# Kernel tuning notes

Hardware: AMD Instinct MI355X
Metric: run time of the kernel (lower is better)

## Reference

```python
import jax, jax.numpy as jnp
import numpy as np

BS, SEQ, DIM, DIM_MLP, E = 2, 2048, 1024, 4096, 8
STD = 0.02  # nn.init.normal_(weight, std=0.02)


def setup_inputs() -> dict:
    key = jax.random.key(0)
    k_x, k_idx, k_w1, k_w2 = jax.random.split(key, 4)
    x = jax.random.normal(k_x, (BS, SEQ, DIM), dtype=jnp.float32)
    expert_idx = jax.random.randint(k_idx, (BS, SEQ), 0, E, dtype=jnp.int32)
    W1 = jax.random.normal(k_w1, (E, DIM, DIM_MLP), dtype=jnp.float32) * STD
    b1 = jnp.zeros((E, DIM_MLP), dtype=jnp.float32)
    W2 = jax.random.normal(k_w2, (E, DIM_MLP, DIM), dtype=jnp.float32) * STD
    b2 = jnp.zeros((E, DIM), dtype=jnp.float32)
    return {"x": x, "expert_idx": expert_idx, "W1": W1, "b1": b1, "W2": W2, "b2": b2}


def reference(x, expert_idx, W1, b1, W2, b2):
    # Compute ALL experts on all tokens (faithful to the torch module).
    # h: [bs, seq, E, dim_mlp]
    h = jnp.einsum("bsd,edm->bsem", x, W1) + b1
    h = jax.nn.gelu(h, approximate=False)  # torch nn.GELU default = exact erf
    # feat: [bs, seq, E, dim]  (== torch.cat along feature dim, reshaped)
    feat = jnp.einsum("bsem,emd->bsed", h, W2) + b2
    # Per-token gather of the assigned expert's output (top-1 select).
    idx = expert_idx.astype(jnp.int32)[:, :, None, None]  # [bs, seq, 1, 1]
    out = jnp.take_along_axis(feat, idx, axis=2)[:, :, 0, :]  # [bs, seq, dim]
    return out
```

## Files before the change

kernel.cpp:

```cpp
#include <hip/hip_runtime.h>
#include <hip/hip_bf16.h>
#include <math.h>

#define TOK   4096
#define DIM   1024
#define DMLP  4096
#define NE    8
#define BM    128
#define BN    128
#define BN2   64
#define BK    64
#define PADMAX (TOK + NE * BM)
#define NTILES (PADMAX / BM)

typedef __attribute__((ext_vector_type(8))) short  short8;
typedef __attribute__((ext_vector_type(4))) float  float4v;
typedef __attribute__((ext_vector_type(4))) unsigned short ushort4v;

#define ASYNC16(gp, lp) __builtin_amdgcn_global_load_lds( \
    (const __attribute__((address_space(1))) unsigned int*)(gp), \
    (__attribute__((address_space(3))) unsigned int*)(lp), 16, 0, 0)

#define FRAG_OFF(R, C) (((((R) << 3) + ((C) ^ ((R) & 7)))) << 3)

static __device__ __forceinline__ unsigned short f2bf(float f) {
  unsigned u = __float_as_uint(f);
  u += 0x7fffu + ((u >> 16) & 1u);
  return (unsigned short)(u >> 16);
}

__global__ void group_kernel(const int* __restrict__ eidx,
                             int* __restrict__ perm,
                             int* __restrict__ tile_e) {
  __shared__ int cnt[NE], off[NE], len[NE], cur[NE];
  const int tid = threadIdx.x;
  if (tid < NE) cnt[tid] = 0;
  __syncthreads();
  for (int i = tid; i < TOK; i += 256) atomicAdd(&cnt[eidx[i]], 1);
  __syncthreads();
  if (tid == 0) {
    int o = 0;
    for (int e = 0; e < NE; e++) {
      off[e] = o;
      len[e] = ((cnt[e] + BM - 1) / BM) * BM;
      cur[e] = o;
      o += len[e];
    }
  }
  __syncthreads();
  for (int s = tid; s < PADMAX; s += 256) perm[s] = -1;
  __syncthreads();
  for (int i = tid; i < TOK; i += 256) {
    const int e = eidx[i];
    const int p = atomicAdd(&cur[e], 1);
    perm[p] = i;
  }
  __syncthreads();
  for (int t = tid; t < NTILES; t += 256) {
    const int row = t * BM;
    int te = -1;
    for (int e = 0; e < NE; e++)
      if (row >= off[e] && row < off[e] + len[e]) te = e;
    tile_e[t] = te;
  }
}

__global__ __launch_bounds__(256)
void convtrans_kernel(const float* __restrict__ W, unsigned short* __restrict__ WT,
                      int K, int N) {
  __shared__ unsigned short T[64][66];
  const int e  = blockIdx.z;
  const int k0 = blockIdx.y * 64, n0 = blockIdx.x * 64;
  const float* Win = W + (size_t)e * K * N;
  unsigned short* Wout = WT + (size_t)e * K * N;
  const int tid = threadIdx.x;
  const int nl  = tid & 63;
  const int kb  = (tid >> 6) * 16;
#pragma unroll
  for (int r = 0; r < 16; r++) {
    const int kl = kb + r;
    T[nl][kl] = f2bf(Win[(size_t)(k0 + kl) * N + n0 + nl]);
  }
  __syncthreads();
  const int kc = (tid & 31) * 2;
  const int nb = tid >> 5;
#pragma unroll
  for (int r = 0; r < 8; r++) {
    const int nl2 = nb + r * 8;
    const unsigned v = *(const unsigned*)&T[nl2][kc];
    *(unsigned*)&Wout[(size_t)(n0 + nl2) * K + k0 + kc] = v;
  }
}

__global__ __launch_bounds__(256)
void xgather_kernel(const float* __restrict__ x, const int* __restrict__ perm,
                    unsigned short* __restrict__ xg) {
  const int slot = blockIdx.x;
  const int t    = perm[slot];
  const int tid  = threadIdx.x;
  ushort4v o = (ushort4v){0, 0, 0, 0};
  if (t >= 0) {
    const float4v v = *(const float4v*)(x + (size_t)t * DIM + tid * 4);
#pragma unroll
    for (int q = 0; q < 4; q++) o[q] = f2bf(v[q]);
  }
  *(ushort4v*)(xg + (size_t)slot * DIM + tid * 4) = o;
}

__global__ __launch_bounds__(256)
void gemm1_kernel(const unsigned short* __restrict__ xg,
                  const unsigned short* __restrict__ W1T,
                  const float* __restrict__ b1, const int* __restrict__ tile_e,
                  unsigned short* __restrict__ h) {
  const int te = tile_e[blockIdx.x];
  if (te < 0) return;
  const unsigned short* Asrc = xg + (size_t)blockIdx.x * BM * DIM;
  const unsigned short* Bsrc = W1T + (size_t)te * DIM * DMLP + (size_t)(blockIdx.y * BN) * DIM;
  const int tid = threadIdx.x;

  __shared__ __align__(16) unsigned short As[BM * BK];
  __shared__ __align__(16) unsigned short Bs[BN * BK];

  const unsigned short* ag[4];
  const unsigned short* bg[4];
  int lo[4];
#pragma unroll
  for (int t = 0; t < 4; t++) {
    const int p = t * 256 + tid;
    const int r = p >> 3;
    const int c = (p & 7) ^ (r & 7);
    ag[t] = Asrc + (size_t)r * DIM + c * 8;
    bg[t] = Bsrc + (size_t)r * DIM + c * 8;
    lo[t] = p * 8;
  }

  const int wid = tid >> 6, lane = tid & 63;
  const int wm = (wid >> 1) * 64, wn = (wid & 1) * 64;
  const int l15 = lane & 15, quad = lane >> 4;

  float4v acc[4][4];
#pragma unroll
  for (int i = 0; i < 4; i++)
#pragma unroll
    for (int j = 0; j < 4; j++) acc[i][j] = (float4v){0.f, 0.f, 0.f, 0.f};

  for (int k0 = 0; k0 < DIM; k0 += BK) {
#pragma unroll
    for (int t = 0; t < 4; t++) ASYNC16(ag[t] + k0, &As[lo[t]]);
#pragma unroll
    for (int t = 0; t < 4; t++) ASYNC16(bg[t] + k0, &Bs[lo[t]]);
    __syncthreads();

#pragma unroll
    for (int hh = 0; hh < 2; hh++) {
      short8 a[4], b[4];
      const int C = hh * 4 + quad;
#pragma unroll
      for (int i = 0; i < 4; i++) a[i] = *(const short8*)&As[FRAG_OFF(wm + i * 16 + l15, C)];
#pragma unroll
      for (int j = 0; j < 4; j++) b[j] = *(const short8*)&Bs[FRAG_OFF(wn + j * 16 + l15, C)];
#pragma unroll
      for (int i = 0; i < 4; i++)
#pragma unroll
        for (int j = 0; j < 4; j++)
          acc[i][j] = __builtin_amdgcn_mfma_f32_16x16x32_bf16(a[i], b[j], acc[i][j], 0, 0, 0);
    }
    __syncthreads();
  }

#pragma unroll
  for (int i = 0; i < 4; i++) {
#pragma unroll
    for (int j = 0; j < 4; j++) {
      const int col = blockIdx.y * BN + wn + j * 16 + l15;
      const float bias = b1[te * DMLP + col];
#pragma unroll
      for (int r = 0; r < 4; r++) {
        const int row = wm + i * 16 + quad * 4 + r;
        float v = acc[i][j][r] + bias;
        v = 0.5f * v * (1.0f + erff(v * 0.7071067811865475f));
        h[(size_t)(blockIdx.x * BM + row) * DMLP + col] = f2bf(v);
      }
    }
  }
}

__global__ __launch_bounds__(256)
void gemm2_kernel(const unsigned short* __restrict__ h,
                  const unsigned short* __restrict__ W2T,
                  const float* __restrict__ b2, const int* __restrict__ perm,
                  const int* __restrict__ tile_e, float* __restrict__ out) {
  const int te = tile_e[blockIdx.x];
  if (te < 0) return;
  const unsigned short* Asrc = h + (size_t)blockIdx.x * BM * DMLP;
  const unsigned short* Bsrc = W2T + (size_t)te * DMLP * DIM + (size_t)(blockIdx.y * BN2) * DMLP;
  const int tid = threadIdx.x;

  __shared__ __align__(16) unsigned short As[BM * BK];
  __shared__ __align__(16) unsigned short Bs[BN2 * BK];

  const unsigned short* ag[4];
  const unsigned short* bg[2];
  int alo[4], blo[2];
#pragma unroll
  for (int t = 0; t < 4; t++) {
    const int p = t * 256 + tid;
    const int r = p >> 3;
    const int c = (p & 7) ^ (r & 7);
    ag[t] = Asrc + (size_t)r * DMLP + c * 8;
    alo[t] = p * 8;
  }
#pragma unroll
  for (int t = 0; t < 2; t++) {
    const int p = t * 256 + tid;
    const int r = p >> 3;
    const int c = (p & 7) ^ (r & 7);
    bg[t] = Bsrc + (size_t)r * DMLP + c * 8;
    blo[t] = p * 8;
  }

  const int wid = tid >> 6, lane = tid & 63;
  const int wm = (wid >> 1) * 64, wn = (wid & 1) * 32;
  const int l15 = lane & 15, quad = lane >> 4;

  float4v acc[4][2];
#pragma unroll
  for (int i = 0; i < 4; i++)
#pragma unroll
    for (int j = 0; j < 2; j++) acc[i][j] = (float4v){0.f, 0.f, 0.f, 0.f};

  for (int k0 = 0; k0 < DMLP; k0 += BK) {
#pragma unroll
    for (int t = 0; t < 4; t++) ASYNC16(ag[t] + k0, &As[alo[t]]);
#pragma unroll
    for (int t = 0; t < 2; t++) ASYNC16(bg[t] + k0, &Bs[blo[t]]);
    __syncthreads();

#pragma unroll
    for (int hh = 0; hh < 2; hh++) {
      short8 a[4], b[2];
      const int C = hh * 4 + quad;
#pragma unroll
      for (int i = 0; i < 4; i++) a[i] = *(const short8*)&As[FRAG_OFF(wm + i * 16 + l15, C)];
#pragma unroll
      for (int j = 0; j < 2; j++) b[j] = *(const short8*)&Bs[FRAG_OFF(wn + j * 16 + l15, C)];
#pragma unroll
      for (int i = 0; i < 4; i++)
#pragma unroll
        for (int j = 0; j < 2; j++)
          acc[i][j] = __builtin_amdgcn_mfma_f32_16x16x32_bf16(a[i], b[j], acc[i][j], 0, 0, 0);
    }
    __syncthreads();
  }

#pragma unroll
  for (int i = 0; i < 4; i++) {
#pragma unroll
    for (int j = 0; j < 2; j++) {
      const int col = blockIdx.y * BN2 + wn + j * 16 + l15;
      const float bias = b2[te * DIM + col];
#pragma unroll
      for (int r = 0; r < 4; r++) {
        const int row  = wm + i * 16 + quad * 4 + r;
        const int slot = blockIdx.x * BM + row;
        const int t    = perm[slot];
        if (t >= 0) out[(size_t)t * DIM + col] = acc[i][j][r] + bias;
      }
    }
  }
}

extern "C" void kernel_launch(void* const* d_in, const int* in_sizes, int n_in,
                              void* d_out, int out_size, void* d_ws, size_t ws_size,
                              hipStream_t stream) {
  const float* x    = (const float*)d_in[0];
  const int*   eidx = (const int*)d_in[1];
  const float* W1   = (const float*)d_in[2];
  const float* b1   = (const float*)d_in[3];
  const float* W2   = (const float*)d_in[4];
  const float* b2   = (const float*)d_in[5];
  float* out = (float*)d_out;

  char* ws = (char*)d_ws;
  int* perm   = (int*)ws;
  int* tile_e = (int*)(ws + PADMAX * sizeof(int));
  unsigned short* xg  = (unsigned short*)(ws + 32768);
  unsigned short* h   = (unsigned short*)(ws + 32768 + 10485760);
  unsigned short* W1T = (unsigned short*)(ws + 32768 + 10485760 + 41943040);
  unsigned short* W2T = (unsigned short*)((char*)W1T + 67108864);

  group_kernel<<<1, 256, 0, stream>>>(eidx, perm, tile_e);
  convtrans_kernel<<<dim3(DMLP / 64, DIM / 64, NE), 256, 0, stream>>>(W1, W1T, DIM, DMLP);
  convtrans_kernel<<<dim3(DIM / 64, DMLP / 64, NE), 256, 0, stream>>>(W2, W2T, DMLP, DIM);
  xgather_kernel<<<PADMAX, 256, 0, stream>>>(x, perm, xg);
  gemm1_kernel<<<dim3(NTILES, DMLP / BN), 256, 0, stream>>>(xg, W1T, b1, tile_e, h);
  gemm2_kernel<<<dim3(NTILES, DIM / BN2), 256, 0, stream>>>(h, W2T, b2, perm, tile_e, out);
}
```

Measured before the change: 494.0 us.

## Pack weights in k8-blocked layout, double-buffer GEMM LDS loads, swap grid order

Replaces the transpose-through-LDS weight conversion with a vectorized pack kernel that writes bf16 weights in [K/8][N][8] blocked order, so the GEMM B-tile loads read contiguous 16-byte chunks. Both GEMMs now double-buffer the A and B tiles in LDS, issuing the next tile's async loads before computing on the current one, with one barrier per iteration. The grid is reordered so consecutive blocks share the same token tile and expert, which should improve L2 reuse of A and the expert weights. The cost is twice the LDS use per block, which may lower occupancy.

```diff
diff --git a/kernel.cpp b/kernel.cpp
--- a/kernel.cpp
+++ b/kernel.cpp
@@ -66,29 +66,22 @@
 }
 
 __global__ __launch_bounds__(256)
-void convtrans_kernel(const float* __restrict__ W, unsigned short* __restrict__ WT,
-                      int K, int N) {
-  __shared__ unsigned short T[64][66];
+void convpack_kernel(const float* __restrict__ W, unsigned short* __restrict__ WT,
+                     int K, int N) {
   const int e  = blockIdx.z;
-  const int k0 = blockIdx.y * 64, n0 = blockIdx.x * 64;
-  const float* Win = W + (size_t)e * K * N;
-  unsigned short* Wout = WT + (size_t)e * K * N;
-  const int tid = threadIdx.x;
-  const int nl  = tid & 63;
-  const int kb  = (tid >> 6) * 16;
-#pragma unroll
-  for (int r = 0; r < 16; r++) {
-    const int kl = kb + r;
-    T[nl][kl] = f2bf(Win[(size_t)(k0 + kl) * N + n0 + nl]);
-  }
-  __syncthreads();
-  const int kc = (tid & 31) * 2;
-  const int nb = tid >> 5;
-#pragma unroll
-  for (int r = 0; r < 8; r++) {
-    const int nl2 = nb + r * 8;
-    const unsigned v = *(const unsigned*)&T[nl2][kc];
-    *(unsigned*)&Wout[(size_t)(n0 + nl2) * K + k0 + kc] = v;
+  const int kg = blockIdx.y;
+  const int n0 = blockIdx.x * 1024 + threadIdx.x * 4;
+  const float* Win = W + (size_t)e * K * N + (size_t)kg * 8 * N + n0;
+  unsigned short* Wout = WT + (size_t)e * K * N + ((size_t)kg * N + n0) * 8;
+  float4v v[8];
+#pragma unroll
+  for (int j = 0; j < 8; j++) v[j] = *(const float4v*)(Win + (size_t)j * N);
+#pragma unroll
+  for (int q = 0; q < 4; q++) {
+    short8 g;
+#pragma unroll
+    for (int j = 0; j < 8; j++) g[j] = (short)f2bf(v[j][q]);
+    *(short8*)(Wout + q * 8) = g;
   }
 }
 
@@ -112,14 +105,16 @@
                   const unsigned short* __restrict__ W1T,
                   const float* __restrict__ b1, const int* __restrict__ tile_e,
                   unsigned short* __restrict__ h) {
-  const int te = tile_e[blockIdx.x];
+  const int bt = blockIdx.y;
+  const int te = tile_e[bt];
   if (te < 0) return;
-  const unsigned short* Asrc = xg + (size_t)blockIdx.x * BM * DIM;
-  const unsigned short* Bsrc = W1T + (size_t)te * DIM * DMLP + (size_t)(blockIdx.y * BN) * DIM;
+  const int n0 = blockIdx.x * BN;
+  const unsigned short* Asrc = xg + (size_t)bt * BM * DIM;
+  const unsigned short* Bsrc = W1T + (size_t)te * DIM * DMLP;
   const int tid = threadIdx.x;
 
-  __shared__ __align__(16) unsigned short As[BM * BK];
-  __shared__ __align__(16) unsigned short Bs[BN * BK];
+  __shared__ __align__(16) unsigned short As[2][BM * BK];
+  __shared__ __align__(16) unsigned short Bs[2][BN * BK];
 
   const unsigned short* ag[4];
   const unsigned short* bg[4];
@@ -130,7 +125,7 @@
     const int r = p >> 3;
     const int c = (p & 7) ^ (r & 7);
     ag[t] = Asrc + (size_t)r * DIM + c * 8;
-    bg[t] = Bsrc + (size_t)r * DIM + c * 8;
+    bg[t] = Bsrc + ((size_t)c * DMLP + n0 + r) * 8;
     lo[t] = p * 8;
   }
 
@@ -144,45 +139,66 @@
 #pragma unroll
     for (int j = 0; j < 4; j++) acc[i][j] = (float4v){0.f, 0.f, 0.f, 0.f};
 
-  for (int k0 = 0; k0 < DIM; k0 += BK) {
-#pragma unroll
-    for (int t = 0; t < 4; t++) ASYNC16(ag[t] + k0, &As[lo[t]]);
-#pragma unroll
-    for (int t = 0; t < 4; t++) ASYNC16(bg[t] + k0, &Bs[lo[t]]);
-    __syncthreads();
-
-#pragma unroll
-    for (int hh = 0; hh < 2; hh++) {
-      short8 a[4], b[4];
-      const int C = hh * 4 + quad;
-#pragma unroll
-      for (int i = 0; i < 4; i++) a[i] = *(const short8*)&As[FRAG_OFF(wm + i * 16 + l15, C)];
-#pragma unroll
-      for (int j = 0; j < 4; j++) b[j] = *(const short8*)&Bs[FRAG_OFF(wn + j * 16 + l15, C)];
-#pragma unroll
-      for (int i = 0; i < 4; i++)
-#pragma unroll
-        for (int j = 0; j < 4; j++)
-          acc[i][j] = __builtin_amdgcn_mfma_f32_16x16x32_bf16(a[i], b[j], acc[i][j], 0, 0, 0);
-    }
-    __syncthreads();
-  }
+#define COMPUTE1(buf)                                                          \
+  do {                                                                         \
+    _Pragma("unroll")                                                          \
+    for (int hh = 0; hh < 2; hh++) {                                           \
+      short8 a[4], b[4];                                                       \
+      const int C = hh * 4 + quad;                                             \
+      _Pragma("unroll")                                                        \
+      for (int i = 0; i < 4; i++)                                              \
+        a[i] = *(const short8*)&As[buf][FRAG_OFF(wm + i * 16 + l15, C)];       \
+      _Pragma("unroll")                                                        \
+      for (int j = 0; j < 4; j++)                                              \
+        b[j] = *(const short8*)&Bs[buf][FRAG_OFF(wn + j * 16 + l15, C)];       \
+      _Pragma("unroll")                                                        \
+      for (int i = 0; i < 4; i++)                                              \
+        _Pragma("unroll")                                                      \
+        for (int j = 0; j < 4; j++)                                            \
+          acc[i][j] = __builtin_amdgcn_mfma_f32_16x16x32_bf16(a[i], b[j],      \
+                                                              acc[i][j], 0, 0, 0); \
+    }                                                                          \
+  } while (0)
+
+#pragma unroll
+  for (int t = 0; t < 4; t++) ASYNC16(ag[t], &As[0][lo[t]]);
+#pragma unroll
+  for (int t = 0; t < 4; t++) ASYNC16(bg[t], &Bs[0][lo[t]]);
+  asm volatile("s_waitcnt vmcnt(0)" ::: "memory");
+  __builtin_amdgcn_s_barrier();
+  __builtin_amdgcn_sched_barrier(0);
+
+  int cur = 0;
+  for (int k0 = BK; k0 < DIM; k0 += BK) {
+    const int nxt = cur ^ 1;
+#pragma unroll
+    for (int t = 0; t < 4; t++) ASYNC16(ag[t] + k0, &As[nxt][lo[t]]);
+#pragma unroll
+    for (int t = 0; t < 4; t++) ASYNC16(bg[t] + (size_t)k0 * DMLP, &Bs[nxt][lo[t]]);
+    COMPUTE1(cur);
+    asm volatile("s_waitcnt vmcnt(0)" ::: "memory");
+    __builtin_amdgcn_s_barrier();
+    __builtin_amdgcn_sched_barrier(0);
+    cur = nxt;
+  }
+  COMPUTE1(cur);
 
 #pragma unroll
   for (int i = 0; i < 4; i++) {
 #pragma unroll
     for (int j = 0; j < 4; j++) {
-      const int col = blockIdx.y * BN + wn + j * 16 + l15;
+      const int col = n0 + wn + j * 16 + l15;
       const float bias = b1[te * DMLP + col];
 #pragma unroll
       for (int r = 0; r < 4; r++) {
         const int row = wm + i * 16 + quad * 4 + r;
         float v = acc[i][j][r] + bias;
         v = 0.5f * v * (1.0f + erff(v * 0.7071067811865475f));
-        h[(size_t)(blockIdx.x * BM + row) * DMLP + col] = f2bf(v);
+        h[(size_t)(bt * BM + row) * DMLP + col] = f2bf(v);
       }
     }
   }
+#undef COMPUTE1
 }
 
 __global__ __launch_bounds__(256)
@@ -190,14 +206,16 @@
                   const unsigned short* __restrict__ W2T,
                   const float* __restrict__ b2, const int* __restrict__ perm,
                   const int* __restrict__ tile_e, float* __restrict__ out) {
-  const int te = tile_e[blockIdx.x];
+  const int bt = blockIdx.y;
+  const int te = tile_e[bt];
   if (te < 0) return;
-  const unsigned short* Asrc = h + (size_t)blockIdx.x * BM * DMLP;
-  const unsigned short* Bsrc = W2T + (size_t)te * DMLP * DIM + (size_t)(blockIdx.y * BN2) * DMLP;
+  const int n0 = blockIdx.x * BN2;
+  const unsigned short* Asrc = h + (size_t)bt * BM * DMLP;
+  const unsigned short* Bsrc = W2T + (size_t)te * DMLP * DIM;
   const int tid = threadIdx.x;
 
-  __shared__ __align__(16) unsigned short As[BM * BK];
-  __shared__ __align__(16) unsigned short Bs[BN2 * BK];
+  __shared__ __align__(16) unsigned short As[2][BM * BK];
+  __shared__ __align__(16) unsigned short Bs[2][BN2 * BK];
 
   const unsigned short* ag[4];
   const unsigned short* bg[2];
@@ -215,7 +233,7 @@
     const int p = t * 256 + tid;
     const int r = p >> 3;
     const int c = (p & 7) ^ (r & 7);
-    bg[t] = Bsrc + (size_t)r * DMLP + c * 8;
+    bg[t] = Bsrc + ((size_t)c * DIM + n0 + r) * 8;
     blo[t] = p * 8;
   }
 
@@ -229,45 +247,66 @@
 #pragma unroll
     for (int j = 0; j < 2; j++) acc[i][j] = (float4v){0.f, 0.f, 0.f, 0.f};
 
-  for (int k0 = 0; k0 < DMLP; k0 += BK) {
-#pragma unroll
-    for (int t = 0; t < 4; t++) ASYNC16(ag[t] + k0, &As[alo[t]]);
-#pragma unroll
-    for (int t = 0; t < 2; t++) ASYNC16(bg[t] + k0, &Bs[blo[t]]);
-    __syncthreads();
-
-#pragma unroll
-    for (int hh = 0; hh < 2; hh++) {
-      short8 a[4], b[2];
-      const int C = hh * 4 + quad;
-#pragma unroll
-      for (int i = 0; i < 4; i++) a[i] = *(const short8*)&As[FRAG_OFF(wm + i * 16 + l15, C)];
-#pragma unroll
-      for (int j = 0; j < 2; j++) b[j] = *(const short8*)&Bs[FRAG_OFF(wn + j * 16 + l15, C)];
-#pragma unroll
-      for (int i = 0; i < 4; i++)
-#pragma unroll
-        for (int j = 0; j < 2; j++)
-          acc[i][j] = __builtin_amdgcn_mfma_f32_16x16x32_bf16(a[i], b[j], acc[i][j], 0, 0, 0);
-    }
-    __syncthreads();
-  }
+#define COMPUTE2(buf)                                                          \
+  do {                                                                         \
+    _Pragma("unroll")                                                          \
+    for (int hh = 0; hh < 2; hh++) {                                           \
+      short8 a[4], b[2];                                                       \
+      const int C = hh * 4 + quad;                                             \
+      _Pragma("unroll")                                                        \
+      for (int i = 0; i < 4; i++)                                              \
+        a[i] = *(const short8*)&As[buf][FRAG_OFF(wm + i * 16 + l15, C)];       \
+      _Pragma("unroll")                                                        \
+      for (int j = 0; j < 2; j++)                                              \
+        b[j] = *(const short8*)&Bs[buf][FRAG_OFF(wn + j * 16 + l15, C)];       \
+      _Pragma("unroll")                                                        \
+      for (int i = 0; i < 4; i++)                                              \
+        _Pragma("unroll")                                                      \
+        for (int j = 0; j < 2; j++)                                            \
+          acc[i][j] = __builtin_amdgcn_mfma_f32_16x16x32_bf16(a[i], b[j],      \
+                                                              acc[i][j], 0, 0, 0); \
+    }                                                                          \
+  } while (0)
+
+#pragma unroll
+  for (int t = 0; t < 4; t++) ASYNC16(ag[t], &As[0][alo[t]]);
+#pragma unroll
+  for (int t = 0; t < 2; t++) ASYNC16(bg[t], &Bs[0][blo[t]]);
+  asm volatile("s_waitcnt vmcnt(0)" ::: "memory");
+  __builtin_amdgcn_s_barrier();
+  __builtin_amdgcn_sched_barrier(0);
+
+  int cur = 0;
+  for (int k0 = BK; k0 < DMLP; k0 += BK) {
+    const int nxt = cur ^ 1;
+#pragma unroll
+    for (int t = 0; t < 4; t++) ASYNC16(ag[t] + k0, &As[nxt][alo[t]]);
+#pragma unroll
+    for (int t = 0; t < 2; t++) ASYNC16(bg[t] + (size_t)k0 * DIM, &Bs[nxt][blo[t]]);
+    COMPUTE2(cur);
+    asm volatile("s_waitcnt vmcnt(0)" ::: "memory");
+    __builtin_amdgcn_s_barrier();
+    __builtin_amdgcn_sched_barrier(0);
+    cur = nxt;
+  }
+  COMPUTE2(cur);
 
 #pragma unroll
   for (int i = 0; i < 4; i++) {
 #pragma unroll
     for (int j = 0; j < 2; j++) {
-      const int col = blockIdx.y * BN2 + wn + j * 16 + l15;
+      const int col = n0 + wn + j * 16 + l15;
       const float bias = b2[te * DIM + col];
 #pragma unroll
       for (int r = 0; r < 4; r++) {
         const int row  = wm + i * 16 + quad * 4 + r;
-        const int slot = blockIdx.x * BM + row;
+        const int slot = bt * BM + row;
         const int t    = perm[slot];
         if (t >= 0) out[(size_t)t * DIM + col] = acc[i][j][r] + bias;
       }
     }
   }
+#undef COMPUTE2
 }
 
 extern "C" void kernel_launch(void* const* d_in, const int* in_sizes, int n_in,
@@ -290,9 +329,9 @@
   unsigned short* W2T = (unsigned short*)((char*)W1T + 67108864);
 
   group_kernel<<<1, 256, 0, stream>>>(eidx, perm, tile_e);
-  convtrans_kernel<<<dim3(DMLP / 64, DIM / 64, NE), 256, 0, stream>>>(W1, W1T, DIM, DMLP);
-  convtrans_kernel<<<dim3(DIM / 64, DMLP / 64, NE), 256, 0, stream>>>(W2, W2T, DMLP, DIM);
+  convpack_kernel<<<dim3(DMLP / 1024, DIM / 8, NE), 256, 0, stream>>>(W1, W1T, DIM, DMLP);
+  convpack_kernel<<<dim3(DIM / 1024, DMLP / 8, NE), 256, 0, stream>>>(W2, W2T, DMLP, DIM);
   xgather_kernel<<<PADMAX, 256, 0, stream>>>(x, perm, xg);
-  gemm1_kernel<<<dim3(NTILES, DMLP / BN), 256, 0, stream>>>(xg, W1T, b1, tile_e, h);
-  gemm2_kernel<<<dim3(NTILES, DIM / BN2), 256, 0, stream>>>(h, W2T, b2, perm, tile_e, out);
-}
+  gemm1_kernel<<<dim3(DMLP / BN, NTILES), 256, 0, stream>>>(xg, W1T, b1, tile_e, h);
+  gemm2_kernel<<<dim3(DIM / BN2, NTILES), 256, 0, stream>>>(h, W2T, b2, perm, tile_e, out);
+}
```

Result: slower. 556.0 us (+12.6%).
